# Kernel optimization log

Measured on AMD Instinct MI355X. Metric: run time of the kernel, lower is better.

The kernel has to match this reference:

```python
import jax, jax.numpy as jnp
import numpy as np

HIDDEN = 96
INF = 1e30


def setup_inputs() -> dict:
    key = jax.random.key(0)
    ks = jax.random.split(key, 9)
    B, JX, JM, D_IN, D_MEM = 8, 2048, 2048, 150, 150
    GATED = D_IN + D_MEM  # 300
    inputs = jax.random.normal(ks[0], (B, JX, D_IN), dtype=jnp.float32)
    memory = jax.random.normal(ks[1], (B, JM, D_MEM), dtype=jnp.float32)
    mask = jax.random.randint(ks[2], (B, JM), 0, 2, dtype=jnp.int32)
    s_in = 1.0 / np.sqrt(D_IN)
    s_g = 1.0 / np.sqrt(GATED)
    Wi = jax.random.uniform(ks[3], (D_IN, HIDDEN), jnp.float32, -s_in, s_in)
    bi = jax.random.uniform(ks[4], (HIDDEN,), jnp.float32, -s_in, s_in)
    Wm = jax.random.uniform(ks[5], (D_MEM, HIDDEN), jnp.float32, -s_in, s_in)
    bm = jax.random.uniform(ks[6], (HIDDEN,), jnp.float32, -s_in, s_in)
    Wg = jax.random.uniform(ks[7], (GATED, GATED), jnp.float32, -s_g, s_g)
    bg = jax.random.uniform(ks[8], (GATED,), jnp.float32, -s_g, s_g)
    return {"inputs": inputs, "memory": memory, "mask": mask,
            "Wi": Wi, "bi": bi, "Wm": Wm, "bm": bm, "Wg": Wg, "bg": bg}


def reference(inputs, memory, mask, Wi, bi, Wm, bm, Wg, bg):
    # ReLU projections (inference mode: dropout is identity)
    inputs_ = jax.nn.relu(jnp.einsum('bxd,dh->bxh', inputs, Wi) + bi)  # [B,JX,H]
    memory_ = jax.nn.relu(jnp.einsum('byd,dh->byh', memory, Wm) + bm)  # [B,JM,H]
    # Scaled dot-product scores [B,JX,JM]
    scores = jnp.einsum('bxh,byh->bxy', inputs_, memory_) / jnp.sqrt(
        jnp.asarray(HIDDEN, inputs.dtype))
    # Additive mask: -INF where mask==0 (broadcast over JX)
    maskf = mask.astype(inputs.dtype)[:, None, :]  # [B,1,JM]
    scores = scores - INF * (1.0 - maskf)
    logits = jax.nn.softmax(scores, axis=-1)
    outputs = jnp.einsum('bxy,byd->bxd', logits, memory)  # [B,JX,D_MEM]
    res = jnp.concatenate([inputs, outputs], axis=2)  # [B,JX,GATED]
    gate = jax.nn.sigmoid(jnp.einsum('bxg,gk->bxk', res, Wg) + bg)
    return gate * res
```

## Files before the change

### kernel.cpp

```cpp
#include <hip/hip_runtime.h>

#define BB 8
#define JX 2048
#define JMDIM 2048
#define DID 150
#define HID 96
#define GATED 300
#define NSPLIT 4
#define NROWS (BB * JX)

typedef unsigned short u16;
typedef __attribute__((ext_vector_type(8))) short bh8;
typedef __attribute__((ext_vector_type(4))) float f32x4;

#define SCALE2    (0.14724444f)

__device__ inline float b2f(u16 u) {
    union { unsigned int i; float f; } c; c.i = ((unsigned int)u) << 16; return c.f;
}
__device__ inline u16 f2b(float f) {
    unsigned int u = __float_as_uint(f);
    unsigned int r = (u + 0x7fffu + ((u >> 16) & 1u)) >> 16;
    return (u16)r;
}

__global__ __launch_bounds__(256) void prep_kernel(
    const float* __restrict__ Wi, const float* __restrict__ Wm,
    const float* __restrict__ Wg, const int* __restrict__ mask,
    u16* __restrict__ Wti, u16* __restrict__ Wtm, u16* __restrict__ Wgt,
    int* __restrict__ idx, int* __restrict__ mcount) {
    if (blockIdx.x >= 128) {
        __shared__ int wsum[4];
        int b = blockIdx.x - 128;
        int tid = threadIdx.x;
        const int* m = mask + (size_t)b * JMDIM;
        int v[8], cnt = 0;
#pragma unroll
        for (int k = 0; k < 8; ++k) { v[k] = m[tid * 8 + k]; cnt += v[k]; }
        int lane = tid & 63, wave = tid >> 6;
        int sc = cnt;
        for (int off = 1; off < 64; off <<= 1) {
            int t = __shfl_up(sc, off, 64);
            if (lane >= off) sc += t;
        }
        if (lane == 63) wsum[wave] = sc;
        __syncthreads();
        int wbase = 0;
        for (int w = 0; w < wave; ++w) wbase += wsum[w];
        int base = wbase + sc - cnt;
        int* ib = idx + (size_t)b * JMDIM;
#pragma unroll
        for (int k = 0; k < 8; ++k) if (v[k]) ib[base++] = tid * 8 + k;
        if (tid == 255) mcount[b] = base;
        return;
    }
    int tid = blockIdx.x * 256 + threadIdx.x;
    const int nthr = 128 * 256;
    for (int e = tid; e < 96 * 168; e += nthr) {
        int h = e / 168, d = e - h * 168;
        Wti[e] = (d < DID) ? f2b(Wi[d * HID + h]) : (u16)0;
        Wtm[e] = (d < DID) ? f2b(Wm[d * HID + h]) : (u16)0;
    }
    for (int e = tid; e < 304 * 328; e += nthr) {
        int k = e / 328, d = e - k * 328;
        Wgt[e] = (k < GATED && d < GATED) ? f2b(Wg[d * GATED + k]) : (u16)0;
    }
}

__global__ __launch_bounds__(256) void projq_kernel(
    const float* __restrict__ inputs, const u16* __restrict__ Wti,
    const float* __restrict__ bi,
    u16* __restrict__ Qp, u16* __restrict__ Xi) {
    __shared__ __align__(16) u16 Xl[64 * 168];
    __shared__ __align__(16) u16 Wl[96 * 168];
    int tid = threadIdx.x;
    size_t row0 = (size_t)blockIdx.x * 64;

    const float4* Xv = (const float4*)(inputs + row0 * DID);
    for (int i = tid; i < 2400; i += 256) {
        float4 v = Xv[i];
        int base = i * 4;
#pragma unroll
        for (int k = 0; k < 4; ++k) {
            int id = base + k;
            int r = id / DID, d = id - r * DID;
            Xl[r * 168 + d] = f2b(((const float*)&v)[k]);
        }
    }
    for (int e = tid; e < 64 * 18; e += 256) {
        int r = e / 18, d = 150 + (e - r * 18);
        Xl[r * 168 + d] = 0;
    }
    for (int i = tid; i < 96 * 21; i += 256) {
        *(bh8*)(Wl + i * 8) = *(const bh8*)(Wti + i * 8);
    }
    __syncthreads();

    for (int e = tid; e < 64 * 20; e += 256) {
        int r = e / 20, c = e - r * 20;
        *(bh8*)(Xi + (row0 + r) * 160 + c * 8) = *(const bh8*)(Xl + r * 168 + c * 8);
    }

    int wave = tid >> 6, lane = tid & 63, quad = lane >> 4, l15 = lane & 15;
    bh8 af[5];
#pragma unroll
    for (int kc = 0; kc < 5; ++kc)
        af[kc] = *(const bh8*)(Xl + (wave * 16 + l15) * 168 + kc * 32 + quad * 8);
#pragma unroll
    for (int nt = 0; nt < 6; ++nt) {
        f32x4 acc = {0.f, 0.f, 0.f, 0.f};
#pragma unroll
        for (int kc = 0; kc < 5; ++kc) {
            bh8 bf = *(const bh8*)(Wl + (nt * 16 + l15) * 168 + kc * 32 + quad * 8);
            acc = __builtin_amdgcn_mfma_f32_16x16x32_bf16(af[kc], bf, acc, 0, 0, 0);
        }
        int h = nt * 16 + l15;
        float bv = bi[h];
#pragma unroll
        for (int j = 0; j < 4; ++j) {
            float y = acc[j] + bv;
            y = y > 0.f ? y : 0.f;
            Qp[(row0 + wave * 16 + quad * 4 + j) * HID + h] = f2b(y);
        }
    }
}

__global__ __launch_bounds__(256) void projkv_kernel(
    const float* __restrict__ memory, const u16* __restrict__ Wtm,
    const float* __restrict__ bm, const int* __restrict__ idx,
    const int* __restrict__ mcount,
    u16* __restrict__ Kp, u16* __restrict__ Vt) {
    __shared__ __align__(16) u16 Xl[64 * 168];
    __shared__ __align__(16) u16 Wl[96 * 168];
    __shared__ int Il[64];
    const int b = blockIdx.y, s = blockIdx.x;
    const int mc = mcount[b];
    const int ntiles = (mc + 63) >> 6;
    if (s >= ntiles) return;
    const int tid = threadIdx.x;
    const int jc0 = s * 64;

    if (tid < 64) {
        int jc = jc0 + tid;
        Il[tid] = (jc < mc) ? idx[(size_t)b * JMDIM + jc] : -1;
    }
    for (int i = tid; i < 96 * 21; i += 256) {
        *(bh8*)(Wl + i * 8) = *(const bh8*)(Wtm + i * 8);
    }
    __syncthreads();

    const float* Mb = memory + (size_t)b * JMDIM * DID;
    for (int e = tid; e < 64 * 75; e += 256) {
        int r = e / 75, c = e - r * 75;
        int row = Il[r];
        float2 val = make_float2(0.f, 0.f);
        if (row >= 0) val = *(const float2*)(Mb + (size_t)row * DID + c * 2);
        Xl[r * 168 + c * 2]     = f2b(val.x);
        Xl[r * 168 + c * 2 + 1] = f2b(val.y);
    }
    for (int e = tid; e < 64 * 18; e += 256) {
        int r = e / 18, d = 150 + (e - r * 18);
        Xl[r * 168 + d] = 0;
    }
    __syncthreads();

    for (int e = tid; e < 160 * 64; e += 256) {
        int d = e >> 6, c = e & 63;
        int jc = jc0 + c;
        u16 v;
        if (d < DID)       v = Xl[c * 168 + d];
        else if (d == DID) v = (jc < mc) ? (u16)0x3F80 : (u16)0;
        else               v = 0;
        Vt[((size_t)b * 160 + d) * JMDIM + jc] = v;
    }

    int wave = tid >> 6, lane = tid & 63, quad = lane >> 4, l15 = lane & 15;
    bh8 af[5];
#pragma unroll
    for (int kc = 0; kc < 5; ++kc)
        af[kc] = *(const bh8*)(Xl + (wave * 16 + l15) * 168 + kc * 32 + quad * 8);
#pragma unroll
    for (int nt = 0; nt < 6; ++nt) {
        f32x4 acc = {0.f, 0.f, 0.f, 0.f};
#pragma unroll
        for (int kc = 0; kc < 5; ++kc) {
            bh8 bf = *(const bh8*)(Wl + (nt * 16 + l15) * 168 + kc * 32 + quad * 8);
            acc = __builtin_amdgcn_mfma_f32_16x16x32_bf16(af[kc], bf, acc, 0, 0, 0);
        }
        int h = nt * 16 + l15;
        float bv = bm[h];
#pragma unroll
        for (int j = 0; j < 4; ++j) {
            float y = acc[j] + bv;
            y = y > 0.f ? y : 0.f;
            Kp[((size_t)b * JMDIM + jc0 + wave * 16 + quad * 4 + j) * HID + h] = f2b(y);
        }
    }
}

template <int SPLIT>
__global__ __launch_bounds__(256, 2) void attn_kernel(
    const u16* __restrict__ Qp, const u16* __restrict__ Kp,
    const u16* __restrict__ Vt, const int* __restrict__ mcount,
    u16* __restrict__ Opart, float* __restrict__ lpart) {
    __shared__ __align__(16) u16 Kl[64 * 104];
    __shared__ __align__(16) u16 Vl[160 * 72];
    __shared__ __align__(16) u16 Pl[128 * 72];
    const int b = blockIdx.y;
    const int x0 = blockIdx.x * 128;
    const int tid = threadIdx.x;
    const int wave = tid >> 6, lane = tid & 63;
    const int quad = lane >> 4, l15 = lane & 15;

    const int mc = mcount[b];
    const int ntiles = (mc + 63) >> 6;
    const int zi = blockIdx.z;
    const int myT = (ntiles > zi) ? ((ntiles - 1 - zi) / SPLIT + 1) : 0;

    bh8 qf[2][3];
#pragma unroll
    for (int mt = 0; mt < 2; ++mt) {
        const u16* qb = Qp + ((size_t)b * JX + x0 + wave * 32 + mt * 16 + l15) * HID + quad * 8;
        qf[mt][0] = *(const bh8*)(qb);
        qf[mt][1] = *(const bh8*)(qb + 32);
        qf[mt][2] = *(const bh8*)(qb + 64);
    }

    f32x4 o[2][10];
    const f32x4 zero4 = {0.f, 0.f, 0.f, 0.f};
#pragma unroll
    for (int mt = 0; mt < 2; ++mt)
#pragma unroll
        for (int i = 0; i < 10; ++i) o[mt][i] = zero4;

    const int jm0_0 = zi * 64;

    const u16* kptr[3]; u16* kdst[3];
#pragma unroll
    for (int t = 0; t < 3; ++t) {
        int i = tid + t * 256, r = i / 12, c = i - r * 12;
        kptr[t] = Kp + ((size_t)b * JMDIM + jm0_0 + r) * HID + c * 8;
        kdst[t] = Kl + r * 104 + c * 8;
    }
    const u16* vptr[5]; u16* vdst[5];
#pragma unroll
    for (int t = 0; t < 5; ++t) {
        int i = tid + t * 256, d = i >> 3, c = i & 7;
        vptr[t] = Vt + ((size_t)b * 160 + d) * JMDIM + jm0_0 + c * 8;
        vdst[t] = Vl + d * 72 + c * 8;
    }

    bh8 kreg[3], vreg[5];
    if (myT > 0) {
#pragma unroll
        for (int t = 0; t < 3; ++t) { kreg[t] = *(const bh8*)kptr[t]; kptr[t] += SPLIT * 64 * HID; }
#pragma unroll
        for (int t = 0; t < 5; ++t) { vreg[t] = *(const bh8*)vptr[t]; vptr[t] += SPLIT * 64; }
    }

    for (int it = 0; it < myT; ++it) {
        __syncthreads();
#pragma unroll
        for (int t = 0; t < 3; ++t) *(bh8*)kdst[t] = kreg[t];
#pragma unroll
        for (int t = 0; t < 5; ++t) *(bh8*)vdst[t] = vreg[t];
        if (it + 1 < myT) {
#pragma unroll
            for (int t = 0; t < 3; ++t) { kreg[t] = *(const bh8*)kptr[t]; kptr[t] += SPLIT * 64 * HID; }
#pragma unroll
            for (int t = 0; t < 5; ++t) { vreg[t] = *(const bh8*)vptr[t]; vptr[t] += SPLIT * 64; }
        }
        __syncthreads();

        f32x4 s[2][4];
#pragma unroll
        for (int mt = 0; mt < 2; ++mt)
#pragma unroll
            for (int nt = 0; nt < 4; ++nt) s[mt][nt] = zero4;
#pragma unroll
        for (int nt = 0; nt < 4; ++nt) {
#pragma unroll
            for (int kc = 0; kc < 3; ++kc) {
                bh8 bf = *(const bh8*)(Kl + (nt * 16 + l15) * 104 + kc * 32 + quad * 8);
                s[0][nt] = __builtin_amdgcn_mfma_f32_16x16x32_bf16(qf[0][kc], bf, s[0][nt], 0, 0, 0);
                s[1][nt] = __builtin_amdgcn_mfma_f32_16x16x32_bf16(qf[1][kc], bf, s[1][nt], 0, 0, 0);
            }
        }
#pragma unroll
        for (int nt = 0; nt < 4; ++nt) {
#pragma unroll
            for (int mt = 0; mt < 2; ++mt)
#pragma unroll
                for (int j = 0; j < 4; ++j) {
                    float p = exp2f(s[mt][nt][j] * SCALE2);
                    Pl[(wave * 32 + mt * 16 + quad * 4 + j) * 72 + nt * 16 + l15] = f2b(p);
                }
        }
        __threadfence_block();

        bh8 pf[2][2];
#pragma unroll
        for (int mt = 0; mt < 2; ++mt) {
            pf[mt][0] = *(const bh8*)(Pl + (wave * 32 + mt * 16 + l15) * 72 + quad * 8);
            pf[mt][1] = *(const bh8*)(Pl + (wave * 32 + mt * 16 + l15) * 72 + 32 + quad * 8);
        }
#pragma unroll
        for (int nt = 0; nt < 10; ++nt) {
#pragma unroll
            for (int kc = 0; kc < 2; ++kc) {
                bh8 bf = *(const bh8*)(Vl + (nt * 16 + l15) * 72 + kc * 32 + quad * 8);
                o[0][nt] = __builtin_amdgcn_mfma_f32_16x16x32_bf16(pf[0][kc], bf, o[0][nt], 0, 0, 0);
                o[1][nt] = __builtin_amdgcn_mfma_f32_16x16x32_bf16(pf[1][kc], bf, o[1][nt], 0, 0, 0);
            }
        }
    }

    const size_t z = blockIdx.z;
    const int srcLane = (lane & 48) | 6;
#pragma unroll
    for (int mt = 0; mt < 2; ++mt) {
        float lv[4], inv[4];
#pragma unroll
        for (int j = 0; j < 4; ++j) {
            lv[j] = __shfl(o[mt][9][j], srcLane, 64);
            inv[j] = (lv[j] > 0.f) ? 1.f / lv[j] : 0.f;
        }
        size_t grow = (size_t)b * JX + x0 + wave * 32 + mt * 16;
#pragma unroll
        for (int nt = 0; nt < 10; ++nt) {
            int d = nt * 16 + l15;
            if (d < 152) {
#pragma unroll
                for (int j = 0; j < 4; ++j)
                    Opart[(z * NROWS + grow + quad * 4 + j) * 152 + d] = f2b(o[mt][nt][j] * inv[j]);
            }
        }
        if (l15 == 0) {
#pragma unroll
            for (int j = 0; j < 4; ++j)
                lpart[z * NROWS + grow + quad * 4 + j] = lv[j];
        }
    }
}

template <int SPLIT>
__global__ __launch_bounds__(256) void gate_kernel(
    const u16* __restrict__ Xi, const u16* __restrict__ Opart,
    const float* __restrict__ lpart,
    const u16* __restrict__ Wgt, const float* __restrict__ bg,
    float* __restrict__ out) {
    __shared__ __align__(16) u16 Rl[16 * 328];
    __shared__ float Cw[SPLIT * 16];
    int tid = threadIdx.x;
    size_t row0 = (size_t)blockIdx.x * 16;

    if (tid < 16) {
        float l[SPLIT], L = 0.f;
#pragma unroll
        for (int s = 0; s < SPLIT; ++s) {
            l[s] = lpart[(size_t)s * NROWS + row0 + tid];
            L += l[s];
        }
        float invL = (L > 0.f) ? 1.f / L : 0.f;
#pragma unroll
        for (int s = 0; s < SPLIT; ++s) Cw[s * 16 + tid] = l[s] * invL;
    }
    for (int e = tid; e < 16 * 20; e += 256) {
        int r = e / 20, c = e - r * 20;
        *(bh8*)(Rl + r * 328 + c * 8) = *(const bh8*)(Xi + (row0 + r) * 160 + c * 8);
    }
    __syncthreads();
    for (int e = tid; e < 16 * 19; e += 256) {
        int r = e / 19, q = e - r * 19;
        float acc[8];
#pragma unroll
        for (int k = 0; k < 8; ++k) acc[k] = 0.f;
#pragma unroll
        for (int s = 0; s < SPLIT; ++s) {
            bh8 v = *(const bh8*)(Opart + ((size_t)s * NROWS + row0 + r) * 152 + q * 8);
            float w = Cw[s * 16 + r];
#pragma unroll
            for (int k = 0; k < 8; ++k) acc[k] += b2f(((const u16*)&v)[k]) * w;
        }
        u16* dst = Rl + r * 328 + 150 + q * 8;
#pragma unroll
        for (int k = 0; k < 8; ++k) dst[k] = f2b(acc[k]);
    }
    for (int e = tid; e < 16 * 26; e += 256) {
        int r = e / 26, c = 302 + (e - r * 26);
        Rl[r * 328 + c] = 0;
    }
    __syncthreads();

    int wave = tid >> 6, lane = tid & 63, quad = lane >> 4, l15 = lane & 15;
    bh8 af[10];
#pragma unroll
    for (int kc = 0; kc < 10; ++kc)
        af[kc] = *(const bh8*)(Rl + l15 * 328 + kc * 32 + quad * 8);
    for (int nt = wave; nt < 19; nt += 4) {
        int h = nt * 16 + l15;
        f32x4 acc = {0.f, 0.f, 0.f, 0.f};
#pragma unroll
        for (int kc = 0; kc < 10; ++kc) {
            bh8 bf = *(const bh8*)(Wgt + (size_t)h * 328 + kc * 32 + quad * 8);
            acc = __builtin_amdgcn_mfma_f32_16x16x32_bf16(af[kc], bf, acc, 0, 0, 0);
        }
        if (h < GATED) {
            float bv = bg[h];
#pragma unroll
            for (int j = 0; j < 4; ++j) {
                int r = quad * 4 + j;
                float x = acc[j] + bv;
                float g = 1.f / (1.f + __expf(-x));
                float rv = b2f(Rl[r * 328 + h]);
                out[(row0 + r) * GATED + h] = g * rv;
            }
        }
    }
}

extern "C" void kernel_launch(void* const* d_in, const int* in_sizes, int n_in,
                              void* d_out, int out_size, void* d_ws, size_t ws_size,
                              hipStream_t stream) {
    const float* inputs = (const float*)d_in[0];
    const float* memory = (const float*)d_in[1];
    const int*   mask   = (const int*)d_in[2];
    const float* Wi = (const float*)d_in[3];
    const float* bi = (const float*)d_in[4];
    const float* Wm = (const float*)d_in[5];
    const float* bm = (const float*)d_in[6];
    const float* Wg = (const float*)d_in[7];
    const float* bg = (const float*)d_in[8];
    float* out = (float*)d_out;

    u16* Qp  = (u16*)d_ws;
    u16* Kp  = Qp + (size_t)NROWS * HID;
    u16* Vt  = Kp + (size_t)NROWS * HID;
    u16* Xi  = Vt + (size_t)BB * 160 * JMDIM;
    u16* Wti = Xi + (size_t)NROWS * 160;
    u16* Wtm = Wti + 96 * 168;
    u16* Wgt = Wtm + 96 * 168;
    u16* Opart = Wgt + 304 * 328;
    size_t u16_elems = (size_t)(Opart - Qp) + (size_t)NSPLIT * NROWS * 152;
    size_t base_bytes = ((u16_elems * sizeof(u16)) + 15) & ~(size_t)15;
    float* lpart = (float*)((char*)d_ws + base_bytes);
    int* idx = (int*)(lpart + (size_t)NSPLIT * NROWS);
    int* mcountp = idx + (size_t)BB * JMDIM;
    size_t needed = base_bytes + (size_t)NSPLIT * NROWS * sizeof(float)
                  + (size_t)BB * JMDIM * sizeof(int) + BB * sizeof(int);
    if (ws_size < needed) return;

    prep_kernel<<<dim3(136), 256, 0, stream>>>(Wi, Wm, Wg, mask, Wti, Wtm, Wgt,
                                               idx, mcountp);
    projq_kernel<<<dim3(NROWS / 64), 256, 0, stream>>>(inputs, Wti, bi, Qp, Xi);
    projkv_kernel<<<dim3(32, BB), 256, 0, stream>>>(memory, Wtm, bm, idx, mcountp,
                                                    Kp, Vt);
    attn_kernel<NSPLIT><<<dim3(JX / 128, BB, NSPLIT), 256, 0, stream>>>(
        Qp, Kp, Vt, mcountp, Opart, lpart);
    gate_kernel<NSPLIT><<<dim3(NROWS / 16), 256, 0, stream>>>(
        Xi, Opart, lpart, Wgt, bg, out);
}
```

Measured before the change: 147.8 us.

## Merge projection kernels, halve attention split, widen gate tile to 32 rows

Combines the Q and KV projection kernels into one launch, with blockIdx.y choosing the path, so the two independent projections share a single grid and one launch is saved. Lowers NSPLIT from 4 to 2, which gives the attention kernel fewer blocks, each covering a longer key range, and halves the partial-output traffic merged in the gate kernel. The gate kernel now handles 32 rows per block with two MFMA accumulators, so each Wg fragment loaded is reused across twice as many rows. The risk is lower occupancy and parallelism in the attention kernel with fewer splits.

```diff
diff --git a/kernel.cpp b/kernel.cpp
--- a/kernel.cpp
+++ b/kernel.cpp
@@ -6,7 +6,7 @@
 #define DID 150
 #define HID 96
 #define GATED 300
-#define NSPLIT 4
+#define NSPLIT 2
 #define NROWS (BB * JX)
 
 typedef unsigned short u16;
@@ -67,77 +67,74 @@
     }
 }
 
-__global__ __launch_bounds__(256) void projq_kernel(
-    const float* __restrict__ inputs, const u16* __restrict__ Wti,
-    const float* __restrict__ bi,
-    u16* __restrict__ Qp, u16* __restrict__ Xi) {
-    __shared__ __align__(16) u16 Xl[64 * 168];
-    __shared__ __align__(16) u16 Wl[96 * 168];
-    int tid = threadIdx.x;
-    size_t row0 = (size_t)blockIdx.x * 64;
-
-    const float4* Xv = (const float4*)(inputs + row0 * DID);
-    for (int i = tid; i < 2400; i += 256) {
-        float4 v = Xv[i];
-        int base = i * 4;
-#pragma unroll
-        for (int k = 0; k < 4; ++k) {
-            int id = base + k;
-            int r = id / DID, d = id - r * DID;
-            Xl[r * 168 + d] = f2b(((const float*)&v)[k]);
-        }
-    }
-    for (int e = tid; e < 64 * 18; e += 256) {
-        int r = e / 18, d = 150 + (e - r * 18);
-        Xl[r * 168 + d] = 0;
-    }
-    for (int i = tid; i < 96 * 21; i += 256) {
-        *(bh8*)(Wl + i * 8) = *(const bh8*)(Wti + i * 8);
-    }
-    __syncthreads();
-
-    for (int e = tid; e < 64 * 20; e += 256) {
-        int r = e / 20, c = e - r * 20;
-        *(bh8*)(Xi + (row0 + r) * 160 + c * 8) = *(const bh8*)(Xl + r * 168 + c * 8);
-    }
-
-    int wave = tid >> 6, lane = tid & 63, quad = lane >> 4, l15 = lane & 15;
-    bh8 af[5];
-#pragma unroll
-    for (int kc = 0; kc < 5; ++kc)
-        af[kc] = *(const bh8*)(Xl + (wave * 16 + l15) * 168 + kc * 32 + quad * 8);
-#pragma unroll
-    for (int nt = 0; nt < 6; ++nt) {
-        f32x4 acc = {0.f, 0.f, 0.f, 0.f};
-#pragma unroll
-        for (int kc = 0; kc < 5; ++kc) {
-            bh8 bf = *(const bh8*)(Wl + (nt * 16 + l15) * 168 + kc * 32 + quad * 8);
-            acc = __builtin_amdgcn_mfma_f32_16x16x32_bf16(af[kc], bf, acc, 0, 0, 0);
-        }
-        int h = nt * 16 + l15;
-        float bv = bi[h];
-#pragma unroll
-        for (int j = 0; j < 4; ++j) {
-            float y = acc[j] + bv;
-            y = y > 0.f ? y : 0.f;
-            Qp[(row0 + wave * 16 + quad * 4 + j) * HID + h] = f2b(y);
-        }
-    }
-}
-
-__global__ __launch_bounds__(256) void projkv_kernel(
-    const float* __restrict__ memory, const u16* __restrict__ Wtm,
-    const float* __restrict__ bm, const int* __restrict__ idx,
-    const int* __restrict__ mcount,
+__global__ __launch_bounds__(256) void proj2_kernel(
+    const float* __restrict__ inputs, const float* __restrict__ memory,
+    const u16* __restrict__ Wti, const u16* __restrict__ Wtm,
+    const float* __restrict__ bi, const float* __restrict__ bm,
+    const int* __restrict__ idx, const int* __restrict__ mcount,
+    u16* __restrict__ Qp, u16* __restrict__ Xi,
     u16* __restrict__ Kp, u16* __restrict__ Vt) {
     __shared__ __align__(16) u16 Xl[64 * 168];
     __shared__ __align__(16) u16 Wl[96 * 168];
     __shared__ int Il[64];
-    const int b = blockIdx.y, s = blockIdx.x;
+    const int tid = threadIdx.x;
+
+    if (blockIdx.y == 0) {
+        size_t row0 = (size_t)blockIdx.x * 64;
+        const float4* Xv = (const float4*)(inputs + row0 * DID);
+        for (int i = tid; i < 2400; i += 256) {
+            float4 v = Xv[i];
+            int base = i * 4;
+#pragma unroll
+            for (int k = 0; k < 4; ++k) {
+                int id = base + k;
+                int r = id / DID, d = id - r * DID;
+                Xl[r * 168 + d] = f2b(((const float*)&v)[k]);
+            }
+        }
+        for (int e = tid; e < 64 * 18; e += 256) {
+            int r = e / 18, d = 150 + (e - r * 18);
+            Xl[r * 168 + d] = 0;
+        }
+        for (int i = tid; i < 96 * 21; i += 256) {
+            *(bh8*)(Wl + i * 8) = *(const bh8*)(Wti + i * 8);
+        }
+        __syncthreads();
+
+        for (int e = tid; e < 64 * 20; e += 256) {
+            int r = e / 20, c = e - r * 20;
+            *(bh8*)(Xi + (row0 + r) * 160 + c * 8) = *(const bh8*)(Xl + r * 168 + c * 8);
+        }
+
+        int wave = tid >> 6, lane = tid & 63, quad = lane >> 4, l15 = lane & 15;
+        bh8 af[5];
+#pragma unroll
+        for (int kc = 0; kc < 5; ++kc)
+            af[kc] = *(const bh8*)(Xl + (wave * 16 + l15) * 168 + kc * 32 + quad * 8);
+#pragma unroll
+        for (int nt = 0; nt < 6; ++nt) {
+            f32x4 acc = {0.f, 0.f, 0.f, 0.f};
+#pragma unroll
+            for (int kc = 0; kc < 5; ++kc) {
+                bh8 bf = *(const bh8*)(Wl + (nt * 16 + l15) * 168 + kc * 32 + quad * 8);
+                acc = __builtin_amdgcn_mfma_f32_16x16x32_bf16(af[kc], bf, acc, 0, 0, 0);
+            }
+            int h = nt * 16 + l15;
+            float bv = bi[h];
+#pragma unroll
+            for (int j = 0; j < 4; ++j) {
+                float y = acc[j] + bv;
+                y = y > 0.f ? y : 0.f;
+                Qp[(row0 + wave * 16 + quad * 4 + j) * HID + h] = f2b(y);
+            }
+        }
+        return;
+    }
+
+    const int b = blockIdx.x >> 5, s = blockIdx.x & 31;
     const int mc = mcount[b];
     const int ntiles = (mc + 63) >> 6;
     if (s >= ntiles) return;
-    const int tid = threadIdx.x;
     const int jc0 = s * 64;
 
     if (tid < 64) {
@@ -349,12 +346,12 @@
     const float* __restrict__ lpart,
     const u16* __restrict__ Wgt, const float* __restrict__ bg,
     float* __restrict__ out) {
-    __shared__ __align__(16) u16 Rl[16 * 328];
-    __shared__ float Cw[SPLIT * 16];
+    __shared__ __align__(16) u16 Rl[32 * 328];
+    __shared__ float Cw[SPLIT * 32];
     int tid = threadIdx.x;
-    size_t row0 = (size_t)blockIdx.x * 16;
-
-    if (tid < 16) {
+    size_t row0 = (size_t)blockIdx.x * 32;
+
+    if (tid < 32) {
         float l[SPLIT], L = 0.f;
 #pragma unroll
         for (int s = 0; s < SPLIT; ++s) {
@@ -363,14 +360,14 @@
         }
         float invL = (L > 0.f) ? 1.f / L : 0.f;
 #pragma unroll
-        for (int s = 0; s < SPLIT; ++s) Cw[s * 16 + tid] = l[s] * invL;
-    }
-    for (int e = tid; e < 16 * 20; e += 256) {
+        for (int s = 0; s < SPLIT; ++s) Cw[s * 32 + tid] = l[s] * invL;
+    }
+    for (int e = tid; e < 32 * 20; e += 256) {
         int r = e / 20, c = e - r * 20;
         *(bh8*)(Rl + r * 328 + c * 8) = *(const bh8*)(Xi + (row0 + r) * 160 + c * 8);
     }
     __syncthreads();
-    for (int e = tid; e < 16 * 19; e += 256) {
+    for (int e = tid; e < 32 * 19; e += 256) {
         int r = e / 19, q = e - r * 19;
         float acc[8];
 #pragma unroll
@@ -378,7 +375,7 @@
 #pragma unroll
         for (int s = 0; s < SPLIT; ++s) {
             bh8 v = *(const bh8*)(Opart + ((size_t)s * NROWS + row0 + r) * 152 + q * 8);
-            float w = Cw[s * 16 + r];
+            float w = Cw[s * 32 + r];
 #pragma unroll
             for (int k = 0; k < 8; ++k) acc[k] += b2f(((const u16*)&v)[k]) * w;
         }
@@ -386,34 +383,41 @@
 #pragma unroll
         for (int k = 0; k < 8; ++k) dst[k] = f2b(acc[k]);
     }
-    for (int e = tid; e < 16 * 26; e += 256) {
+    for (int e = tid; e < 32 * 26; e += 256) {
         int r = e / 26, c = 302 + (e - r * 26);
         Rl[r * 328 + c] = 0;
     }
     __syncthreads();
 
     int wave = tid >> 6, lane = tid & 63, quad = lane >> 4, l15 = lane & 15;
-    bh8 af[10];
-#pragma unroll
-    for (int kc = 0; kc < 10; ++kc)
-        af[kc] = *(const bh8*)(Rl + l15 * 328 + kc * 32 + quad * 8);
+    bh8 af[2][10];
+#pragma unroll
+    for (int mt = 0; mt < 2; ++mt)
+#pragma unroll
+        for (int kc = 0; kc < 10; ++kc)
+            af[mt][kc] = *(const bh8*)(Rl + (mt * 16 + l15) * 328 + kc * 32 + quad * 8);
     for (int nt = wave; nt < 19; nt += 4) {
         int h = nt * 16 + l15;
-        f32x4 acc = {0.f, 0.f, 0.f, 0.f};
+        f32x4 acc0 = {0.f, 0.f, 0.f, 0.f};
+        f32x4 acc1 = {0.f, 0.f, 0.f, 0.f};
 #pragma unroll
         for (int kc = 0; kc < 10; ++kc) {
             bh8 bf = *(const bh8*)(Wgt + (size_t)h * 328 + kc * 32 + quad * 8);
-            acc = __builtin_amdgcn_mfma_f32_16x16x32_bf16(af[kc], bf, acc, 0, 0, 0);
+            acc0 = __builtin_amdgcn_mfma_f32_16x16x32_bf16(af[0][kc], bf, acc0, 0, 0, 0);
+            acc1 = __builtin_amdgcn_mfma_f32_16x16x32_bf16(af[1][kc], bf, acc1, 0, 0, 0);
         }
         if (h < GATED) {
             float bv = bg[h];
 #pragma unroll
             for (int j = 0; j < 4; ++j) {
-                int r = quad * 4 + j;
-                float x = acc[j] + bv;
-                float g = 1.f / (1.f + __expf(-x));
-                float rv = b2f(Rl[r * 328 + h]);
-                out[(row0 + r) * GATED + h] = g * rv;
+                int r0 = quad * 4 + j;
+                float x0 = acc0[j] + bv;
+                float g0 = 1.f / (1.f + __expf(-x0));
+                out[(row0 + r0) * GATED + h] = g0 * b2f(Rl[r0 * 328 + h]);
+                int r1 = r0 + 16;
+                float x1 = acc1[j] + bv;
+                float g1 = 1.f / (1.f + __expf(-x1));
+                out[(row0 + r1) * GATED + h] = g1 * b2f(Rl[r1 * 328 + h]);
             }
         }
     }
@@ -452,11 +456,10 @@
 
     prep_kernel<<<dim3(136), 256, 0, stream>>>(Wi, Wm, Wg, mask, Wti, Wtm, Wgt,
                                                idx, mcountp);
-    projq_kernel<<<dim3(NROWS / 64), 256, 0, stream>>>(inputs, Wti, bi, Qp, Xi);
-    projkv_kernel<<<dim3(32, BB), 256, 0, stream>>>(memory, Wtm, bm, idx, mcountp,
-                                                    Kp, Vt);
+    proj2_kernel<<<dim3(256, 2), 256, 0, stream>>>(
+        inputs, memory, Wti, Wtm, bi, bm, idx, mcountp, Qp, Xi, Kp, Vt);
     attn_kernel<NSPLIT><<<dim3(JX / 128, BB, NSPLIT), 256, 0, stream>>>(
         Qp, Kp, Vt, mcountp, Opart, lpart);
-    gate_kernel<NSPLIT><<<dim3(NROWS / 16), 256, 0, stream>>>(
+    gate_kernel<NSPLIT><<<dim3(NROWS / 32), 256, 0, stream>>>(
         Xi, Opart, lpart, Wgt, bg, out);
 }
```

Result: faster. 141.9 us (-3.9%).
